# Optimization experiments

Hardware: AMD Instinct MI355X
Metric: run time of the kernel (lower is better)

The kernel has to match this reference:

```python
import jax, jax.numpy as jnp
import numpy as np


def setup_inputs() -> dict:
    key = jax.random.key(0)
    B, C, T = 64, 256, 2048
    X = jax.random.normal(key, (B, C, T), dtype=jnp.float32)
    return {"X": X}


def reference(X) -> jnp.ndarray:
    # torch.cov(correction=0) per sample: rows = variables, cols = observations
    T = X.shape[-1]
    Xc = X - jnp.mean(X, axis=-1, keepdims=True)      # [B, C, T]
    cov = jnp.einsum('bct,bdt->bcd', Xc, Xc) / T       # [B, C, C]
    return cov
```

## Files before the change

kernel.cpp:

```cpp
#include <hip/hip_runtime.h>


#define NB 64
#define NC 256
#define NT 2048

typedef __bf16 bf16x8 __attribute__((ext_vector_type(8)));
typedef float  f32x8  __attribute__((ext_vector_type(8)));
typedef float  f32x4  __attribute__((ext_vector_type(4)));

__global__ __launch_bounds__(256) void cov_mfma_kernel(const float* __restrict__ X,
                                                       float* __restrict__ out) {
    const int bid  = blockIdx.x;
    const int xcd  = bid & 7;
    const int s    = bid >> 3;
    const int tile = s & 3;
    const int b    = xcd + 8 * (s >> 2);
    const int tm   = tile >> 1, tn = tile & 1;
    const int row0 = tm * 128, col0 = tn * 128;

    const float* __restrict__ Xb = X + (size_t)b * (NC * NT);

    __shared__ __bf16 sA[128 * 32];
    __shared__ __bf16 sB[128 * 32];

    const int t    = threadIdx.x;
    const int lane = t & 63;
    const int wave = t >> 6;
    const int wm   = wave >> 1, wn = wave & 1;
    const int quad = lane >> 4;
    const int l16  = lane & 15;

    const int srow = t >> 2;
    const int sch  = t & 3;

    const float* gA0 = Xb + (size_t)(row0 + srow)      * NT + sch * 8;
    const float* gA1 = Xb + (size_t)(row0 + srow + 64) * NT + sch * 8;
    const float* gB0 = Xb + (size_t)(col0 + srow)      * NT + sch * 8;
    const float* gB1 = Xb + (size_t)(col0 + srow + 64) * NT + sch * 8;

    __bf16* lA0 = &sA[t * 8];
    __bf16* lA1 = &sA[t * 8 + 2048];
    __bf16* lB0 = &sB[t * 8];
    __bf16* lB1 = &sB[t * 8 + 2048];

    f32x4 acc[4][4];
    f32x4 accRS[4];
    f32x4 accCS[4];
#pragma unroll
    for (int i = 0; i < 4; ++i) {
        accRS[i] = (f32x4){0.f, 0.f, 0.f, 0.f};
        accCS[i] = (f32x4){0.f, 0.f, 0.f, 0.f};
#pragma unroll
        for (int j = 0; j < 4; ++j) acc[i][j] = (f32x4){0.f, 0.f, 0.f, 0.f};
    }

    const bf16x8 ones = {(__bf16)1.0f, (__bf16)1.0f, (__bf16)1.0f, (__bf16)1.0f,
                         (__bf16)1.0f, (__bf16)1.0f, (__bf16)1.0f, (__bf16)1.0f};

    for (int kk = 0; kk < NT; kk += 32) {
        f32x8 vA0 = *(const f32x8*)(gA0 + kk);
        f32x8 vA1 = *(const f32x8*)(gA1 + kk);
        f32x8 vB0 = *(const f32x8*)(gB0 + kk);
        f32x8 vB1 = *(const f32x8*)(gB1 + kk);
        bf16x8 hA0 = __builtin_convertvector(vA0, bf16x8);
        bf16x8 hA1 = __builtin_convertvector(vA1, bf16x8);
        bf16x8 hB0 = __builtin_convertvector(vB0, bf16x8);
        bf16x8 hB1 = __builtin_convertvector(vB1, bf16x8);

        __syncthreads();
        *(bf16x8*)lA0 = hA0;
        *(bf16x8*)lA1 = hA1;
        *(bf16x8*)lB0 = hB0;
        *(bf16x8*)lB1 = hB1;
        __syncthreads();

        bf16x8 aF[4], bF[4];
#pragma unroll
        for (int mt = 0; mt < 4; ++mt)
            aF[mt] = *(const bf16x8*)&sA[(wm * 64 + mt * 16 + l16) * 32 + quad * 8];
#pragma unroll
        for (int nt = 0; nt < 4; ++nt)
            bF[nt] = *(const bf16x8*)&sB[(wn * 64 + nt * 16 + l16) * 32 + quad * 8];

#pragma unroll
        for (int mt = 0; mt < 4; ++mt) {
            accRS[mt] = __builtin_amdgcn_mfma_f32_16x16x32_bf16(aF[mt], ones, accRS[mt], 0, 0, 0);
#pragma unroll
            for (int nt = 0; nt < 4; ++nt)
                acc[mt][nt] = __builtin_amdgcn_mfma_f32_16x16x32_bf16(aF[mt], bF[nt], acc[mt][nt], 0, 0, 0);
        }
#pragma unroll
        for (int nt = 0; nt < 4; ++nt)
            accCS[nt] = __builtin_amdgcn_mfma_f32_16x16x32_bf16(ones, bF[nt], accCS[nt], 0, 0, 0);
    }

    const float invT = 1.0f / NT;
    float* __restrict__ outB = out + (size_t)b * (NC * NC);
#pragma unroll
    for (int nt = 0; nt < 4; ++nt) {
        const int col = col0 + wn * 64 + nt * 16 + l16;
        const float muc = accCS[nt][0] * invT;
#pragma unroll
        for (int mt = 0; mt < 4; ++mt) {
            const int rbase = row0 + wm * 64 + mt * 16 + quad * 4;
#pragma unroll
            for (int r = 0; r < 4; ++r) {
                const float mur = accRS[mt][r] * invT;
                outB[(size_t)(rbase + r) * NC + col] = acc[mt][nt][r] * invT - mur * muc;
            }
        }
    }
}

extern "C" void kernel_launch(void* const* d_in, const int* in_sizes, int n_in,
                              void* d_out, int out_size, void* d_ws, size_t ws_size,
                              hipStream_t stream) {
    const float* X = (const float*)d_in[0];
    float* out = (float*)d_out;
    (void)in_sizes; (void)n_in; (void)out_size; (void)d_ws; (void)ws_size;
    cov_mfma_kernel<<<NB * 4, 256, 0, stream>>>(X, out);
}
```

Baseline: 245.1 us.

## Use 64x64 output tiles, pad LDS rows, and prefetch next K slice

Shrinks each block's output tile from 128x128 to 64x64, which raises the grid from 256 to 1024 blocks so more CUs have work on the GPU. It also pads LDS rows to a 40-element stride to reduce bank conflicts on fragment reads, and issues the global load for the next K slice into registers before the MFMA work on the current one. The cost is more redundant global reads of X per block, since each row strip is reloaded by more tiles, and lower MFMA work per block relative to the loads.

```diff
diff --git a/kernel.cpp b/kernel.cpp
--- a/kernel.cpp
+++ b/kernel.cpp
@@ -4,6 +4,7 @@
 #define NB 64
 #define NC 256
 #define NT 2048
+#define LSTR 40
 
 typedef __bf16 bf16x8 __attribute__((ext_vector_type(8)));
 typedef float  f32x8  __attribute__((ext_vector_type(8)));
@@ -14,15 +15,15 @@
     const int bid  = blockIdx.x;
     const int xcd  = bid & 7;
     const int s    = bid >> 3;
-    const int tile = s & 3;
-    const int b    = xcd + 8 * (s >> 2);
-    const int tm   = tile >> 1, tn = tile & 1;
-    const int row0 = tm * 128, col0 = tn * 128;
+    const int tile = s & 15;
+    const int b    = xcd + 8 * (s >> 4);
+    const int tm   = tile >> 2, tn = tile & 3;
+    const int row0 = tm * 64, col0 = tn * 64;
 
     const float* __restrict__ Xb = X + (size_t)b * (NC * NT);
 
-    __shared__ __bf16 sA[128 * 32];
-    __shared__ __bf16 sB[128 * 32];
+    __shared__ __bf16 sA[64 * LSTR];
+    __shared__ __bf16 sB[64 * LSTR];
 
     const int t    = threadIdx.x;
     const int lane = t & 63;
@@ -33,77 +34,71 @@
 
     const int srow = t >> 2;
     const int sch  = t & 3;
+    const float* gA = Xb + (size_t)(row0 + srow) * NT + sch * 8;
+    const float* gB = Xb + (size_t)(col0 + srow) * NT + sch * 8;
+    __bf16* lA = &sA[srow * LSTR + sch * 8];
+    __bf16* lB = &sB[srow * LSTR + sch * 8];
 
-    const float* gA0 = Xb + (size_t)(row0 + srow)      * NT + sch * 8;
-    const float* gA1 = Xb + (size_t)(row0 + srow + 64) * NT + sch * 8;
-    const float* gB0 = Xb + (size_t)(col0 + srow)      * NT + sch * 8;
-    const float* gB1 = Xb + (size_t)(col0 + srow + 64) * NT + sch * 8;
-
-    __bf16* lA0 = &sA[t * 8];
-    __bf16* lA1 = &sA[t * 8 + 2048];
-    __bf16* lB0 = &sB[t * 8];
-    __bf16* lB1 = &sB[t * 8 + 2048];
-
-    f32x4 acc[4][4];
-    f32x4 accRS[4];
-    f32x4 accCS[4];
+    f32x4 acc[2][2];
+    f32x4 accRS[2];
+    f32x4 accCS[2];
 #pragma unroll
-    for (int i = 0; i < 4; ++i) {
+    for (int i = 0; i < 2; ++i) {
         accRS[i] = (f32x4){0.f, 0.f, 0.f, 0.f};
         accCS[i] = (f32x4){0.f, 0.f, 0.f, 0.f};
 #pragma unroll
-        for (int j = 0; j < 4; ++j) acc[i][j] = (f32x4){0.f, 0.f, 0.f, 0.f};
+        for (int j = 0; j < 2; ++j) acc[i][j] = (f32x4){0.f, 0.f, 0.f, 0.f};
     }
 
     const bf16x8 ones = {(__bf16)1.0f, (__bf16)1.0f, (__bf16)1.0f, (__bf16)1.0f,
                          (__bf16)1.0f, (__bf16)1.0f, (__bf16)1.0f, (__bf16)1.0f};
 
+    f32x8 vA = *(const f32x8*)gA;
+    f32x8 vB = *(const f32x8*)gB;
+
     for (int kk = 0; kk < NT; kk += 32) {
-        f32x8 vA0 = *(const f32x8*)(gA0 + kk);
-        f32x8 vA1 = *(const f32x8*)(gA1 + kk);
-        f32x8 vB0 = *(const f32x8*)(gB0 + kk);
-        f32x8 vB1 = *(const f32x8*)(gB1 + kk);
-        bf16x8 hA0 = __builtin_convertvector(vA0, bf16x8);
-        bf16x8 hA1 = __builtin_convertvector(vA1, bf16x8);
-        bf16x8 hB0 = __builtin_convertvector(vB0, bf16x8);
-        bf16x8 hB1 = __builtin_convertvector(vB1, bf16x8);
+        bf16x8 hA = __builtin_convertvector(vA, bf16x8);
+        bf16x8 hB = __builtin_convertvector(vB, bf16x8);
 
         __syncthreads();
-        *(bf16x8*)lA0 = hA0;
-        *(bf16x8*)lA1 = hA1;
-        *(bf16x8*)lB0 = hB0;
-        *(bf16x8*)lB1 = hB1;
+        *(bf16x8*)lA = hA;
+        *(bf16x8*)lB = hB;
         __syncthreads();
 
-        bf16x8 aF[4], bF[4];
+        if (kk + 32 < NT) {
+            vA = *(const f32x8*)(gA + kk + 32);
+            vB = *(const f32x8*)(gB + kk + 32);
+        }
+
+        bf16x8 aF[2], bF[2];
 #pragma unroll
-        for (int mt = 0; mt < 4; ++mt)
-            aF[mt] = *(const bf16x8*)&sA[(wm * 64 + mt * 16 + l16) * 32 + quad * 8];
+        for (int mt = 0; mt < 2; ++mt)
+            aF[mt] = *(const bf16x8*)&sA[(wm * 32 + mt * 16 + l16) * LSTR + quad * 8];
 #pragma unroll
-        for (int nt = 0; nt < 4; ++nt)
-            bF[nt] = *(const bf16x8*)&sB[(wn * 64 + nt * 16 + l16) * 32 + quad * 8];
+        for (int nt = 0; nt < 2; ++nt)
+            bF[nt] = *(const bf16x8*)&sB[(wn * 32 + nt * 16 + l16) * LSTR + quad * 8];
 
 #pragma unroll
-        for (int mt = 0; mt < 4; ++mt) {
+        for (int mt = 0; mt < 2; ++mt) {
             accRS[mt] = __builtin_amdgcn_mfma_f32_16x16x32_bf16(aF[mt], ones, accRS[mt], 0, 0, 0);
 #pragma unroll
-            for (int nt = 0; nt < 4; ++nt)
+            for (int nt = 0; nt < 2; ++nt)
                 acc[mt][nt] = __builtin_amdgcn_mfma_f32_16x16x32_bf16(aF[mt], bF[nt], acc[mt][nt], 0, 0, 0);
         }
 #pragma unroll
-        for (int nt = 0; nt < 4; ++nt)
+        for (int nt = 0; nt < 2; ++nt)
             accCS[nt] = __builtin_amdgcn_mfma_f32_16x16x32_bf16(ones, bF[nt], accCS[nt], 0, 0, 0);
     }
 
     const float invT = 1.0f / NT;
     float* __restrict__ outB = out + (size_t)b * (NC * NC);
 #pragma unroll
-    for (int nt = 0; nt < 4; ++nt) {
-        const int col = col0 + wn * 64 + nt * 16 + l16;
+    for (int nt = 0; nt < 2; ++nt) {
+        const int col = col0 + wn * 32 + nt * 16 + l16;
         const float muc = accCS[nt][0] * invT;
 #pragma unroll
-        for (int mt = 0; mt < 4; ++mt) {
-            const int rbase = row0 + wm * 64 + mt * 16 + quad * 4;
+        for (int mt = 0; mt < 2; ++mt) {
+            const int rbase = row0 + wm * 32 + mt * 16 + quad * 4;
 #pragma unroll
             for (int r = 0; r < 4; ++r) {
                 const float mur = accRS[mt][r] * invT;
@@ -119,5 +114,5 @@
     const float* X = (const float*)d_in[0];
     float* out = (float*)d_out;
     (void)in_sizes; (void)n_in; (void)out_size; (void)d_ws; (void)ws_size;
-    cov_mfma_kernel<<<NB * 4, 256, 0, stream>>>(X, out);
+    cov_mfma_kernel<<<NB * 16, 256, 0, stream>>>(X, out);
 }
```

After: 218.9 us. 10.7% less time.

## Exploit covariance symmetry with upper-triangle 64x64 tiles and split-K waves

Applied to the files above, without the earlier changes.

Replaces the 4 full 128x128 tiles per batch with the 10 upper-triangular 64x64 tiles, writing each result and its transpose. The two waves per block split the time axis in half and reduce through shared memory. Fragments are loaded straight from global into registers with one-step prefetch, so the LDS staging and its per-iteration barriers are gone. This removes nearly half the MFMA work and raises the block count, at the cost of uncoalesced transposed stores and redundant global reads across tiles.

```diff
diff --git a/kernel.cpp b/kernel.cpp
--- a/kernel.cpp
+++ b/kernel.cpp
@@ -4,49 +4,38 @@
 #define NB 64
 #define NC 256
 #define NT 2048
+#define KITER 32
 
 typedef __bf16 bf16x8 __attribute__((ext_vector_type(8)));
 typedef float  f32x8  __attribute__((ext_vector_type(8)));
 typedef float  f32x4  __attribute__((ext_vector_type(4)));
 
-__global__ __launch_bounds__(256) void cov_mfma_kernel(const float* __restrict__ X,
-                                                       float* __restrict__ out) {
+__global__ __launch_bounds__(128, 2) void cov_kernel(const float* __restrict__ X,
+                                                     float* __restrict__ out) {
     const int bid  = blockIdx.x;
     const int xcd  = bid & 7;
     const int s    = bid >> 3;
-    const int tile = s & 3;
-    const int b    = xcd + 8 * (s >> 2);
-    const int tm   = tile >> 1, tn = tile & 1;
-    const int row0 = tm * 128, col0 = tn * 128;
+    const int b    = xcd + 8 * (s / 10);
+    const int tile = s % 10;
+    int tm, tn;
+    if (tile < 4)      { tm = 0; tn = tile; }
+    else if (tile < 7) { tm = 1; tn = tile - 3; }
+    else if (tile < 9) { tm = 2; tn = tile - 5; }
+    else               { tm = 3; tn = 3; }
+    const int row0 = tm * 64, col0 = tn * 64;
 
     const float* __restrict__ Xb = X + (size_t)b * (NC * NT);
-
-    __shared__ __bf16 sA[128 * 32];
-    __shared__ __bf16 sB[128 * 32];
 
     const int t    = threadIdx.x;
     const int lane = t & 63;
     const int wave = t >> 6;
-    const int wm   = wave >> 1, wn = wave & 1;
     const int quad = lane >> 4;
     const int l16  = lane & 15;
 
-    const int srow = t >> 2;
-    const int sch  = t & 3;
+    const float* baseA = Xb + (size_t)(row0 + l16) * NT + wave * (NT / 2) + quad * 8;
+    const float* baseB = Xb + (size_t)(col0 + l16) * NT + wave * (NT / 2) + quad * 8;
 
-    const float* gA0 = Xb + (size_t)(row0 + srow)      * NT + sch * 8;
-    const float* gA1 = Xb + (size_t)(row0 + srow + 64) * NT + sch * 8;
-    const float* gB0 = Xb + (size_t)(col0 + srow)      * NT + sch * 8;
-    const float* gB1 = Xb + (size_t)(col0 + srow + 64) * NT + sch * 8;
-
-    __bf16* lA0 = &sA[t * 8];
-    __bf16* lA1 = &sA[t * 8 + 2048];
-    __bf16* lB0 = &sB[t * 8];
-    __bf16* lB1 = &sB[t * 8 + 2048];
-
-    f32x4 acc[4][4];
-    f32x4 accRS[4];
-    f32x4 accCS[4];
+    f32x4 acc[4][4], accRS[4], accCS[4];
 #pragma unroll
     for (int i = 0; i < 4; ++i) {
         accRS[i] = (f32x4){0.f, 0.f, 0.f, 0.f};
@@ -58,31 +47,29 @@
     const bf16x8 ones = {(__bf16)1.0f, (__bf16)1.0f, (__bf16)1.0f, (__bf16)1.0f,
                          (__bf16)1.0f, (__bf16)1.0f, (__bf16)1.0f, (__bf16)1.0f};
 
-    for (int kk = 0; kk < NT; kk += 32) {
-        f32x8 vA0 = *(const f32x8*)(gA0 + kk);
-        f32x8 vA1 = *(const f32x8*)(gA1 + kk);
-        f32x8 vB0 = *(const f32x8*)(gB0 + kk);
-        f32x8 vB1 = *(const f32x8*)(gB1 + kk);
-        bf16x8 hA0 = __builtin_convertvector(vA0, bf16x8);
-        bf16x8 hA1 = __builtin_convertvector(vA1, bf16x8);
-        bf16x8 hB0 = __builtin_convertvector(vB0, bf16x8);
-        bf16x8 hB1 = __builtin_convertvector(vB1, bf16x8);
+    f32x8 vA[4], vB[4];
+#pragma unroll
+    for (int i = 0; i < 4; ++i) {
+        vA[i] = *(const f32x8*)(baseA + (size_t)i * 16 * NT);
+        vB[i] = *(const f32x8*)(baseB + (size_t)i * 16 * NT);
+    }
 
-        __syncthreads();
-        *(bf16x8*)lA0 = hA0;
-        *(bf16x8*)lA1 = hA1;
-        *(bf16x8*)lB0 = hB0;
-        *(bf16x8*)lB1 = hB1;
-        __syncthreads();
-
+#pragma unroll 1
+    for (int it = 0; it < KITER; ++it) {
         bf16x8 aF[4], bF[4];
 #pragma unroll
-        for (int mt = 0; mt < 4; ++mt)
-            aF[mt] = *(const bf16x8*)&sA[(wm * 64 + mt * 16 + l16) * 32 + quad * 8];
+        for (int i = 0; i < 4; ++i) {
+            aF[i] = __builtin_convertvector(vA[i], bf16x8);
+            bF[i] = __builtin_convertvector(vB[i], bf16x8);
+        }
+        if (it + 1 < KITER) {
+            const int off = (it + 1) * 32;
 #pragma unroll
-        for (int nt = 0; nt < 4; ++nt)
-            bF[nt] = *(const bf16x8*)&sB[(wn * 64 + nt * 16 + l16) * 32 + quad * 8];
-
+            for (int i = 0; i < 4; ++i) {
+                vA[i] = *(const f32x8*)(baseA + (size_t)i * 16 * NT + off);
+                vB[i] = *(const f32x8*)(baseB + (size_t)i * 16 * NT + off);
+            }
+        }
 #pragma unroll
         for (int mt = 0; mt < 4; ++mt) {
             accRS[mt] = __builtin_amdgcn_mfma_f32_16x16x32_bf16(aF[mt], ones, accRS[mt], 0, 0, 0);
@@ -95,19 +82,51 @@
             accCS[nt] = __builtin_amdgcn_mfma_f32_16x16x32_bf16(ones, bF[nt], accCS[nt], 0, 0, 0);
     }
 
-    const float invT = 1.0f / NT;
-    float* __restrict__ outB = out + (size_t)b * (NC * NC);
+    __shared__ float red[64 * 65];
+    __shared__ float rsum[64];
+    __shared__ float csum[64];
+
+    if (wave == 0) {
 #pragma unroll
-    for (int nt = 0; nt < 4; ++nt) {
-        const int col = col0 + wn * 64 + nt * 16 + l16;
-        const float muc = accCS[nt][0] * invT;
+        for (int mt = 0; mt < 4; ++mt)
+#pragma unroll
+            for (int nt = 0; nt < 4; ++nt)
+#pragma unroll
+                for (int r = 0; r < 4; ++r)
+                    red[(mt * 16 + quad * 4 + r) * 65 + nt * 16 + l16] = acc[mt][nt][r];
+        if (l16 == 0) {
+#pragma unroll
+            for (int mt = 0; mt < 4; ++mt)
+#pragma unroll
+                for (int r = 0; r < 4; ++r)
+                    rsum[mt * 16 + quad * 4 + r] = accRS[mt][r];
+        }
+        if (quad == 0) {
+#pragma unroll
+            for (int nt = 0; nt < 4; ++nt)
+                csum[nt * 16 + l16] = accCS[nt][0];
+        }
+    }
+    __syncthreads();
+
+    if (wave == 1) {
+        const float invT = 1.0f / NT;
+        float* __restrict__ outB = out + (size_t)b * (NC * NC);
 #pragma unroll
         for (int mt = 0; mt < 4; ++mt) {
-            const int rbase = row0 + wm * 64 + mt * 16 + quad * 4;
 #pragma unroll
-            for (int r = 0; r < 4; ++r) {
-                const float mur = accRS[mt][r] * invT;
-                outB[(size_t)(rbase + r) * NC + col] = acc[mt][nt][r] * invT - mur * muc;
+            for (int nt = 0; nt < 4; ++nt) {
+#pragma unroll
+                for (int r = 0; r < 4; ++r) {
+                    const int rl = mt * 16 + quad * 4 + r;
+                    const int cl = nt * 16 + l16;
+                    const float tot = red[rl * 65 + cl] + acc[mt][nt][r];
+                    const float rsT = rsum[rl] + accRS[mt][r];
+                    const float csT = csum[cl] + accCS[nt][0];
+                    const float val = (tot - rsT * csT * invT) * invT;
+                    outB[(size_t)(row0 + rl) * NC + (col0 + cl)] = val;
+                    outB[(size_t)(col0 + cl) * NC + (row0 + rl)] = val;
+                }
             }
         }
     }
@@ -119,5 +138,5 @@
     const float* X = (const float*)d_in[0];
     float* out = (float*)d_out;
     (void)in_sizes; (void)n_in; (void)out_size; (void)d_ws; (void)ws_size;
-    cov_mfma_kernel<<<NB * 4, 256, 0, stream>>>(X, out);
+    cov_kernel<<<640, 128, 0, stream>>>(X, out);
 }
```

After: 240.9 us. Within noise of the previous version (-1.7%).
